# Optimization experiments

Hardware: AMD Instinct MI355X
Metric: run time of the kernel (lower is better)

The kernel has to match this reference:

```python
import jax, jax.numpy as jnp
import numpy as np

D_MODEL = 1024
NUM_HEADS = 16
D_HEAD = D_MODEL // NUM_HEADS


def setup_inputs() -> dict:
    key = jax.random.key(0)
    kx, kq, kk, kv, ko = jax.random.split(key, 5)
    scale = 1.0 / np.sqrt(D_MODEL)
    X = jax.random.normal(kx, (4, 2048, D_MODEL), dtype=jnp.float32)
    # nn.Linear weights stored as [out, in]; we keep that convention.
    W_Q = jax.random.uniform(kq, (D_MODEL, D_MODEL), jnp.float32, -scale, scale)
    W_K = jax.random.uniform(kk, (D_MODEL, D_MODEL), jnp.float32, -scale, scale)
    W_V = jax.random.uniform(kv, (D_MODEL, D_MODEL), jnp.float32, -scale, scale)
    W_O = jax.random.uniform(ko, (D_MODEL, D_MODEL), jnp.float32, -scale, scale)
    return {"X": X, "W_Q": W_Q, "W_K": W_K, "W_V": W_V, "W_O": W_O}


def reference(X, W_Q, W_K, W_V, W_O):
    B, S, D = X.shape
    H, Dh = NUM_HEADS, D_HEAD
    # projections (Linear: x @ W.T)
    Q = (X @ W_Q.T).reshape(B, S, H, Dh).transpose(0, 2, 1, 3)  # [B,H,S,Dh]
    K = (X @ W_K.T).reshape(B, S, H, Dh).transpose(0, 2, 1, 3)
    V = (X @ W_V.T).reshape(B, S, H, Dh).transpose(0, 2, 1, 3)
    scores = jnp.einsum('bhqd,bhkd->bhqk', Q, K) / jnp.sqrt(jnp.float32(Dh))
    causal = jnp.tril(jnp.ones((S, S), dtype=bool))  # True = keep
    scores = jnp.where(causal, scores, -jnp.inf)
    attn = jax.nn.softmax(scores, axis=-1)
    out = jnp.einsum('bhqk,bhkd->bhqd', attn, V)  # [B,H,S,Dh]
    out = out.transpose(0, 2, 1, 3).reshape(B, S, D)
    return out @ W_O.T
```

## Files before the change

kernel.cpp:

```cpp
#include <hip/hip_runtime.h>

#define S_LEN 2048
#define NH 16
#define DH 64
#define DM 1024
#define M_TOK 8192
#define SZX ((size_t)M_TOK * DM)
#define SZW ((size_t)DM * DM)

typedef unsigned short u16;
typedef unsigned int u32;
typedef __attribute__((ext_vector_type(8))) short bf16x8;
typedef __attribute__((ext_vector_type(4))) float f32x4;

__device__ __forceinline__ u16 f2bf(float f) {
  union { float f; u32 u; } v; v.f = f;
  return (u16)((v.u + 0x8000u) >> 16);
}
__device__ __forceinline__ u32 pack_bf2(float x, float y) {
  union { float f; u32 u; } a, b; a.f = x; b.f = y;
  return __builtin_amdgcn_perm(b.u + 0x8000u, a.u + 0x8000u, 0x07060302u);
}
__device__ __forceinline__ float fast_exp2(float x) {
  float r; asm("v_exp_f32 %0, %1" : "=v"(r) : "v"(x)); return r;
}
__device__ __forceinline__ void gload16(const u16* g, u16* l) {
  __builtin_amdgcn_global_load_lds((const __attribute__((address_space(1))) void*)g,
                                   (__attribute__((address_space(3))) void*)l,
                                   16, 0, 0);
}

#define QSCALE 0.18033688f

__global__ __launch_bounds__(256) void cast_all(const float* __restrict__ X,
                                                const float* __restrict__ q,
                                                const float* __restrict__ k,
                                                const float* __restrict__ v,
                                                const float* __restrict__ o,
                                                u16* __restrict__ dst) {
  const int i = (blockIdx.x * 256 + threadIdx.x) * 8;
  const float* src;
  int local;
  if (i < (int)SZX) { src = X; local = i; }
  else {
    const int j = i - (int)SZX;
    const int region = j >> 20;
    src = (region == 0) ? q : (region == 1) ? k : (region == 2) ? v : o;
    local = j & ((1 << 20) - 1);
  }
  const float4 a = *(const float4*)(src + local);
  const float4 b = *(const float4*)(src + local + 4);
  uint4 r;
  r.x = pack_bf2(a.x, a.y); r.y = pack_bf2(a.z, a.w);
  r.z = pack_bf2(b.x, b.y); r.w = pack_bf2(b.z, b.w);
  *(uint4*)(dst + i) = r;
}

template<int MODE, bool SW>
__device__ __forceinline__ void gemm_body(const u16* __restrict__ A,
                                          const u16* __restrict__ Bw,
                                          void* __restrict__ Cv,
                                          u16* __restrict__ As,
                                          u16* __restrict__ Bs) {
  const int tid = threadIdx.x;
  const int lane = tid & 63;
  const int wave = tid >> 6;
  const int col = lane & 15, quad = lane >> 4;
  const int wm = (wave & 1) * 64, wn = (wave >> 1) * 64;
  const int m_blk = blockIdx.x * 128, n_blk = blockIdx.y * 128;

  const int srow = tid >> 3;
  const int skg = (tid & 7) ^ (srow & 7);
  const u16* Ag = A + (size_t)(m_blk + srow) * DM + skg * 8;
  const u16* Bg = Bw + (size_t)(n_blk + srow) * DM + skg * 8;

  f32x4 acc[4][4];
#pragma unroll
  for (int i = 0; i < 4; ++i)
#pragma unroll
    for (int j = 0; j < 4; ++j) acc[i][j] = (f32x4){0.f, 0.f, 0.f, 0.f};

  const int c0 = (quad ^ (col & 7)) * 8;
  const int c1 = c0 ^ 32;

  for (int k0 = 0; k0 < DM; k0 += 64) {
#pragma unroll
    for (int i = 0; i < 4; ++i) {
      gload16(Ag + (size_t)(32 * i) * DM + k0, &As[tid * 8 + i * 2048]);
      gload16(Bg + (size_t)(32 * i) * DM + k0, &Bs[tid * 8 + i * 2048]);
    }
    __syncthreads();
    bf16x8 af[4], bf[4];
#pragma unroll
    for (int i = 0; i < 4; ++i)
      af[i] = *(const bf16x8*)&As[(wm + i * 16 + col) * 64 + c0];
#pragma unroll
    for (int j = 0; j < 4; ++j)
      bf[j] = *(const bf16x8*)&Bs[(wn + j * 16 + col) * 64 + c0];
#pragma unroll
    for (int i = 0; i < 4; ++i)
#pragma unroll
      for (int j = 0; j < 4; ++j)
        acc[i][j] = SW
          ? __builtin_amdgcn_mfma_f32_16x16x32_bf16(bf[j], af[i], acc[i][j], 0, 0, 0)
          : __builtin_amdgcn_mfma_f32_16x16x32_bf16(af[i], bf[j], acc[i][j], 0, 0, 0);
#pragma unroll
    for (int i = 0; i < 4; ++i)
      af[i] = *(const bf16x8*)&As[(wm + i * 16 + col) * 64 + c1];
#pragma unroll
    for (int j = 0; j < 4; ++j)
      bf[j] = *(const bf16x8*)&Bs[(wn + j * 16 + col) * 64 + c1];
#pragma unroll
    for (int i = 0; i < 4; ++i)
#pragma unroll
      for (int j = 0; j < 4; ++j)
        acc[i][j] = SW
          ? __builtin_amdgcn_mfma_f32_16x16x32_bf16(bf[j], af[i], acc[i][j], 0, 0, 0)
          : __builtin_amdgcn_mfma_f32_16x16x32_bf16(af[i], bf[j], acc[i][j], 0, 0, 0);
    __syncthreads();
  }

  if (MODE == 0 && SW) {
    const int which = n_blk >> 10;
    const float sc = (which == 0) ? QSCALE : 1.0f;
    u16* dst = (u16*)Cv + (size_t)which * SZX;
    const int h = ((n_blk + wn) & 1023) >> 6;
#pragma unroll
    for (int i = 0; i < 4; ++i) {
      const int m = m_blk + wm + i * 16 + col;
      const int b = m >> 11, s = m & 2047;
      const size_t rowb = ((size_t)(b * NH + h) * S_LEN + s) * DH;
#pragma unroll
      for (int j = 0; j < 4; ++j) {
        const int dh0 = j * 16 + quad * 4;
        uint2 pk;
        pk.x = pack_bf2(acc[i][j][0] * sc, acc[i][j][1] * sc);
        pk.y = pack_bf2(acc[i][j][2] * sc, acc[i][j][3] * sc);
        *(uint2*)&dst[rowb + dh0] = pk;
      }
    }
  } else if (MODE == 0) {
#pragma unroll
    for (int i = 0; i < 4; ++i) {
#pragma unroll
      for (int j = 0; j < 4; ++j) {
        const int n = n_blk + wn + j * 16 + col;
        const int nn = n & 1023;
        const int h = nn >> 6, dh = nn & 63;
        u16* dst = (u16*)Cv + (size_t)2 * SZX;
        const int m0 = m_blk + wm + i * 16 + quad * 4;
        const int b = m0 >> 11;
        uint2 pk;
        pk.x = pack_bf2(acc[i][j][0], acc[i][j][1]);
        pk.y = pack_bf2(acc[i][j][2], acc[i][j][3]);
        *(uint2*)&dst[((size_t)((b * NH + h) * DH + dh)) * S_LEN + (m0 & 2047)] = pk;
      }
    }
  } else {
#pragma unroll
    for (int i = 0; i < 4; ++i) {
      const int m = m_blk + wm + i * 16 + col;
#pragma unroll
      for (int j = 0; j < 4; ++j) {
        const int n0 = n_blk + wn + j * 16 + quad * 4;
        float4 v;
        v.x = acc[i][j][0]; v.y = acc[i][j][1];
        v.z = acc[i][j][2]; v.w = acc[i][j][3];
        *(float4*)&((float*)Cv)[(size_t)m * DM + n0] = v;
      }
    }
  }
}

template<int MODE>
__global__ __launch_bounds__(256) void gemm128(const u16* __restrict__ A,
                                               const u16* __restrict__ Bw,
                                               void* __restrict__ Cv) {
  __shared__ __align__(16) u16 As[128 * 64];
  __shared__ __align__(16) u16 Bs[128 * 64];
  if (MODE == 0) {
    if ((blockIdx.y * 128) >> 10 == 2) gemm_body<0, false>(A, Bw, Cv, As, Bs);
    else                               gemm_body<0, true >(A, Bw, Cv, As, Bs);
  } else {
    gemm_body<1, true>(A, Bw, Cv, As, Bs);
  }
}

template<bool DIAG_L>
__device__ __forceinline__ void stepM(const u16* __restrict__ Ksb,
                                      const u16* __restrict__ Vsb,
                                      u16* __restrict__ Pw,
                                      bf16x8 qH0, bf16x8 qH1,
                                      bf16x8 qL0, bf16x8 qL1,
                                      f32x4& lH, f32x4* oH,
                                      f32x4& lL, f32x4* oL,
                                      f32x4 zero4, bf16x8 ones,
                                      int c0, int c1, int col, int quad,
                                      int q_l) {
  const int colc = col & 7;
  f32x4 sH[4], sL[4];
#pragma unroll
  for (int t = 0; t < 4; ++t) {
    const int row = (t * 16 + col) * 64;
    const bf16x8 kf0 = *(const bf16x8*)&Ksb[row + c0];
    const bf16x8 kf1 = *(const bf16x8*)&Ksb[row + c1];
    f32x4 z = __builtin_amdgcn_mfma_f32_16x16x32_bf16(kf0, qH0, zero4, 0, 0, 0);
    sH[t] = __builtin_amdgcn_mfma_f32_16x16x32_bf16(kf1, qH1, z, 0, 0, 0);
    f32x4 y = __builtin_amdgcn_mfma_f32_16x16x32_bf16(kf0, qL0, zero4, 0, 0, 0);
    sL[t] = __builtin_amdgcn_mfma_f32_16x16x32_bf16(kf1, qL1, y, 0, 0, 0);
  }
#pragma unroll
  for (int t = 0; t < 4; ++t)
#pragma unroll
    for (int r = 0; r < 4; ++r) {
      sH[t][r] = fast_exp2(sH[t][r]);
      if (DIAG_L && (t * 16 + quad * 4 + r) > q_l) sL[t][r] = -1e30f;
      sL[t][r] = fast_exp2(sL[t][r]);
    }
#pragma unroll
  for (int t = 0; t < 4; ++t) {
    uint2 pk;
    pk.x = pack_bf2(sH[t][0], sH[t][1]);
    pk.y = pack_bf2(sH[t][2], sH[t][3]);
    const int pg = (((t * 2) + (quad >> 1)) ^ colc) * 8 + (quad & 1) * 4;
    *(uint2*)&Pw[col * 64 + pg] = pk;
  }
  const bf16x8 pfH0 = *(const bf16x8*)&Pw[col * 64 + ((quad ^ colc) * 8)];
  const bf16x8 pfH1 = *(const bf16x8*)&Pw[col * 64 + (((4 + quad) ^ colc) * 8)];
#pragma unroll
  for (int t = 0; t < 4; ++t) {
    uint2 pk;
    pk.x = pack_bf2(sL[t][0], sL[t][1]);
    pk.y = pack_bf2(sL[t][2], sL[t][3]);
    const int pg = (((t * 2) + (quad >> 1)) ^ colc) * 8 + (quad & 1) * 4;
    *(uint2*)&Pw[col * 64 + pg] = pk;
  }
  const bf16x8 pfL0 = *(const bf16x8*)&Pw[col * 64 + ((quad ^ colc) * 8)];
  const bf16x8 pfL1 = *(const bf16x8*)&Pw[col * 64 + (((4 + quad) ^ colc) * 8)];
  lH = __builtin_amdgcn_mfma_f32_16x16x32_bf16(ones, pfH0, lH, 0, 0, 0);
  lH = __builtin_amdgcn_mfma_f32_16x16x32_bf16(ones, pfH1, lH, 0, 0, 0);
  lL = __builtin_amdgcn_mfma_f32_16x16x32_bf16(ones, pfL0, lL, 0, 0, 0);
  lL = __builtin_amdgcn_mfma_f32_16x16x32_bf16(ones, pfL1, lL, 0, 0, 0);
#pragma unroll
  for (int t = 0; t < 4; ++t) {
    const int row = (t * 16 + col) * 64;
    const bf16x8 vf0 = *(const bf16x8*)&Vsb[row + c0];
    const bf16x8 vf1 = *(const bf16x8*)&Vsb[row + c1];
    oH[t] = __builtin_amdgcn_mfma_f32_16x16x32_bf16(vf0, pfH0, oH[t], 0, 0, 0);
    oH[t] = __builtin_amdgcn_mfma_f32_16x16x32_bf16(vf1, pfH1, oH[t], 0, 0, 0);
    oL[t] = __builtin_amdgcn_mfma_f32_16x16x32_bf16(vf0, pfL0, oL[t], 0, 0, 0);
    oL[t] = __builtin_amdgcn_mfma_f32_16x16x32_bf16(vf1, pfL1, oL[t], 0, 0, 0);
  }
}

template<bool DIAG_H>
__device__ __forceinline__ void stepS(const u16* __restrict__ Ksb,
                                      const u16* __restrict__ Vsb,
                                      u16* __restrict__ Pw,
                                      bf16x8 qH0, bf16x8 qH1,
                                      f32x4& lH, f32x4* oH,
                                      f32x4 zero4, bf16x8 ones,
                                      int c0, int c1, int col, int quad,
                                      int q_l) {
  const int colc = col & 7;
  f32x4 sH[4];
#pragma unroll
  for (int t = 0; t < 4; ++t) {
    const int row = (t * 16 + col) * 64;
    const bf16x8 kf0 = *(const bf16x8*)&Ksb[row + c0];
    const bf16x8 kf1 = *(const bf16x8*)&Ksb[row + c1];
    f32x4 z = __builtin_amdgcn_mfma_f32_16x16x32_bf16(kf0, qH0, zero4, 0, 0, 0);
    sH[t] = __builtin_amdgcn_mfma_f32_16x16x32_bf16(kf1, qH1, z, 0, 0, 0);
  }
#pragma unroll
  for (int t = 0; t < 4; ++t)
#pragma unroll
    for (int r = 0; r < 4; ++r) {
      if (DIAG_H && (t * 16 + quad * 4 + r) > q_l) sH[t][r] = -1e30f;
      sH[t][r] = fast_exp2(sH[t][r]);
    }
#pragma unroll
  for (int t = 0; t < 4; ++t) {
    uint2 pk;
    pk.x = pack_bf2(sH[t][0], sH[t][1]);
    pk.y = pack_bf2(sH[t][2], sH[t][3]);
    const int pg = (((t * 2) + (quad >> 1)) ^ colc) * 8 + (quad & 1) * 4;
    *(uint2*)&Pw[col * 64 + pg] = pk;
  }
  const bf16x8 pf0 = *(const bf16x8*)&Pw[col * 64 + ((quad ^ colc) * 8)];
  const bf16x8 pf1 = *(const bf16x8*)&Pw[col * 64 + (((4 + quad) ^ colc) * 8)];
  lH = __builtin_amdgcn_mfma_f32_16x16x32_bf16(ones, pf0, lH, 0, 0, 0);
  lH = __builtin_amdgcn_mfma_f32_16x16x32_bf16(ones, pf1, lH, 0, 0, 0);
#pragma unroll
  for (int t = 0; t < 4; ++t) {
    const int row = (t * 16 + col) * 64;
    const bf16x8 vf0 = *(const bf16x8*)&Vsb[row + c0];
    const bf16x8 vf1 = *(const bf16x8*)&Vsb[row + c1];
    oH[t] = __builtin_amdgcn_mfma_f32_16x16x32_bf16(vf0, pf0, oH[t], 0, 0, 0);
    oH[t] = __builtin_amdgcn_mfma_f32_16x16x32_bf16(vf1, pf1, oH[t], 0, 0, 0);
  }
}

__global__ __launch_bounds__(256) void attn_kernel(const u16* __restrict__ Qg,
                                                   const u16* __restrict__ Kg,
                                                   const u16* __restrict__ Vtg,
                                                   u16* __restrict__ AO) {
  __shared__ __align__(16) u16 Ks[2][2][64 * 64];
  __shared__ __align__(16) u16 Vs[2][2][64 * 64];
  __shared__ __align__(16) u16 Ps[4][16 * 64];

  const int id = blockIdx.x;
  const int bh = ((id & 7) << 3) | (id >> 6);
  const int slot = (id >> 3) & 7;
  const int tid = threadIdx.x, lane = tid & 63, wave = tid >> 6;
  const int col = lane & 15, quad = lane >> 4;

  const u16* Qb = Qg + (size_t)bh * S_LEN * DH;
  const u16* Kb = Kg + (size_t)bh * S_LEN * DH;
  const u16* Vb = Vtg + (size_t)bh * DH * S_LEN;

  const f32x4 zero4 = (f32x4){0.f, 0.f, 0.f, 0.f};
  const bf16x8 ones = (bf16x8){0x3F80, 0x3F80, 0x3F80, 0x3F80,
                               0x3F80, 0x3F80, 0x3F80, 0x3F80};

  const int sr0 = tid >> 3;
  const int sk0 = (tid & 7) ^ (sr0 & 7);
  const u16* K0 = Kb + (size_t)sr0 * DH + sk0 * 8;
  const u16* K1 = Kb + (size_t)(sr0 + 32) * DH + sk0 * 8;
  const u16* V0 = Vb + (size_t)sr0 * S_LEN + sk0 * 8;
  const u16* V1 = Vb + (size_t)(sr0 + 32) * S_LEN + sk0 * 8;

  const int c0 = (quad ^ (col & 7)) * 8;
  const int c1 = c0 ^ 32;
  const int q_l = wave * 16 + col;
  u16* Pw = &Ps[wave][0];
  const int b = bh >> 4, h = bh & 15;

#define STAGEW(w, nb) do {                                            \
    gload16(K0 + (size_t)(2 * (w)) * 64 * DH,     &Ks[nb][0][tid * 8]);        \
    gload16(K1 + (size_t)(2 * (w)) * 64 * DH,     &Ks[nb][0][2048 + tid * 8]); \
    gload16(K0 + (size_t)(2 * (w) + 1) * 64 * DH, &Ks[nb][1][tid * 8]);        \
    gload16(K1 + (size_t)(2 * (w) + 1) * 64 * DH, &Ks[nb][1][2048 + tid * 8]); \
    gload16(V0 + (2 * (w)) * 64,                  &Vs[nb][0][tid * 8]);        \
    gload16(V1 + (2 * (w)) * 64,                  &Vs[nb][0][2048 + tid * 8]); \
    gload16(V0 + (2 * (w) + 1) * 64,              &Vs[nb][1][tid * 8]);        \
    gload16(V1 + (2 * (w) + 1) * 64,              &Vs[nb][1][2048 + tid * 8]); \
  } while (0)

  for (int pi = 0; pi < 2; ++pi) {
    const int p = pi ? slot : (15 - slot);
    const int qtH = 2 * p + 1;

    const u16* qrowH = Qb + (size_t)(qtH * 64 + wave * 16 + col) * DH + quad * 8;
    const bf16x8 qH0 = *(const bf16x8*)(qrowH);
    const bf16x8 qH1 = *(const bf16x8*)(qrowH + 32);
    const bf16x8 qL0 = *(const bf16x8*)(qrowH - 64 * DH);
    const bf16x8 qL1 = *(const bf16x8*)(qrowH - 64 * DH + 32);

    f32x4 lH = zero4, lL = zero4;
    f32x4 oH[4], oL[4];
#pragma unroll
    for (int t = 0; t < 4; ++t) { oH[t] = zero4; oL[t] = zero4; }

    __syncthreads();
    STAGEW(0, 0);

    for (int w = 0; w < p; ++w) {
      __syncthreads();
      STAGEW(w + 1, (w + 1) & 1);
      stepM<false>(&Ks[w & 1][0][0], &Vs[w & 1][0][0], Pw,
                   qH0, qH1, qL0, qL1, lH, oH, lL, oL,
                   zero4, ones, c0, c1, col, quad, q_l);
      stepM<false>(&Ks[w & 1][1][0], &Vs[w & 1][1][0], Pw,
                   qH0, qH1, qL0, qL1, lH, oH, lL, oL,
                   zero4, ones, c0, c1, col, quad, q_l);
    }
    {
      __syncthreads();
      stepM<true>(&Ks[p & 1][0][0], &Vs[p & 1][0][0], Pw,
                  qH0, qH1, qL0, qL1, lH, oH, lL, oL,
                  zero4, ones, c0, c1, col, quad, q_l);
      stepS<true>(&Ks[p & 1][1][0], &Vs[p & 1][1][0], Pw,
                  qH0, qH1, lH, oH, zero4, ones, c0, c1, col, quad, q_l);
    }

    {
      const float inv = __builtin_amdgcn_rcpf(lH[0]);
      const size_t base = (size_t)(b * S_LEN + qtH * 64 + q_l) * DM + h * DH;
#pragma unroll
      for (int t = 0; t < 4; ++t) {
        uint2 pk;
        pk.x = pack_bf2(oH[t][0] * inv, oH[t][1] * inv);
        pk.y = pack_bf2(oH[t][2] * inv, oH[t][3] * inv);
        *(uint2*)&AO[base + t * 16 + quad * 4] = pk;
      }
    }
    {
      const float inv = __builtin_amdgcn_rcpf(lL[0]);
      const size_t base = (size_t)(b * S_LEN + (qtH - 1) * 64 + q_l) * DM + h * DH;
#pragma unroll
      for (int t = 0; t < 4; ++t) {
        uint2 pk;
        pk.x = pack_bf2(oL[t][0] * inv, oL[t][1] * inv);
        pk.y = pack_bf2(oL[t][2] * inv, oL[t][3] * inv);
        *(uint2*)&AO[base + t * 16 + quad * 4] = pk;
      }
    }
  }
#undef STAGEW
}

extern "C" void kernel_launch(void* const* d_in, const int* in_sizes, int n_in,
                              void* d_out, int out_size, void* d_ws, size_t ws_size,
                              hipStream_t stream) {
  const float* X  = (const float*)d_in[0];
  const float* Wq = (const float*)d_in[1];
  const float* Wk = (const float*)d_in[2];
  const float* Wv = (const float*)d_in[3];
  const float* Wo = (const float*)d_in[4];

  u16* Xb   = (u16*)d_ws;
  u16* Wqkv = Xb + SZX;
  u16* Wob  = Wqkv + 3 * SZW;
  u16* Qb   = Wob + SZW;
  u16* Kb   = Qb + SZX;
  u16* VT   = Kb + SZX;
  u16* AO   = Xb;

  cast_all<<<(int)((SZX + 4 * SZW) / 8 / 256), 256, 0, stream>>>(X, Wq, Wk, Wv, Wo, Xb);

  gemm128<0><<<dim3(M_TOK / 128, 3 * DM / 128), 256, 0, stream>>>(Xb, Wqkv, Qb);

  attn_kernel<<<dim3(512), 256, 0, stream>>>(Qb, Kb, VT, AO);

  gemm128<1><<<dim3(M_TOK / 128, DM / 128), 256, 0, stream>>>(AO, Wob, d_out);
}
```

Measured before the change: 229.9 us.

## Double-buffer GEMM shared-memory tiles to overlap global loads with MFMA

```diff
diff --git a/kernel.cpp b/kernel.cpp
--- a/kernel.cpp
+++ b/kernel.cpp
@@ -7,6 +7,7 @@
 #define M_TOK 8192
 #define SZX ((size_t)M_TOK * DM)
 #define SZW ((size_t)DM * DM)
+#define NT 16
 
 typedef unsigned short u16;
 typedef unsigned int u32;
@@ -83,20 +84,31 @@
   const int c0 = (quad ^ (col & 7)) * 8;
   const int c1 = c0 ^ 32;
 
-  for (int k0 = 0; k0 < DM; k0 += 64) {
-#pragma unroll
-    for (int i = 0; i < 4; ++i) {
-      gload16(Ag + (size_t)(32 * i) * DM + k0, &As[tid * 8 + i * 2048]);
-      gload16(Bg + (size_t)(32 * i) * DM + k0, &Bs[tid * 8 + i * 2048]);
-    }
+#define STG(t) do {                                                       \
+    const int kk_ = (t) * 64;                                             \
+    u16* Ad_ = As + ((t) & 1) * 8192;                                     \
+    u16* Bd_ = Bs + ((t) & 1) * 8192;                                     \
+    _Pragma("unroll")                                                     \
+    for (int i_ = 0; i_ < 4; ++i_) {                                      \
+      gload16(Ag + (size_t)(32 * i_) * DM + kk_, &Ad_[tid * 8 + i_ * 2048]); \
+      gload16(Bg + (size_t)(32 * i_) * DM + kk_, &Bd_[tid * 8 + i_ * 2048]); \
+    }                                                                     \
+  } while (0)
+
+  STG(0);
+#pragma unroll 2
+  for (int t = 0; t < NT; ++t) {
     __syncthreads();
+    if (t + 1 < NT) STG(t + 1);
+    const u16* Ab = As + (t & 1) * 8192;
+    const u16* Bb = Bs + (t & 1) * 8192;
     bf16x8 af[4], bf[4];
 #pragma unroll
     for (int i = 0; i < 4; ++i)
-      af[i] = *(const bf16x8*)&As[(wm + i * 16 + col) * 64 + c0];
+      af[i] = *(const bf16x8*)&Ab[(wm + i * 16 + col) * 64 + c0];
 #pragma unroll
     for (int j = 0; j < 4; ++j)
-      bf[j] = *(const bf16x8*)&Bs[(wn + j * 16 + col) * 64 + c0];
+      bf[j] = *(const bf16x8*)&Bb[(wn + j * 16 + col) * 64 + c0];
 #pragma unroll
     for (int i = 0; i < 4; ++i)
 #pragma unroll
@@ -106,10 +118,10 @@
           : __builtin_amdgcn_mfma_f32_16x16x32_bf16(af[i], bf[j], acc[i][j], 0, 0, 0);
 #pragma unroll
     for (int i = 0; i < 4; ++i)
-      af[i] = *(const bf16x8*)&As[(wm + i * 16 + col) * 64 + c1];
+      af[i] = *(const bf16x8*)&Ab[(wm + i * 16 + col) * 64 + c1];
 #pragma unroll
     for (int j = 0; j < 4; ++j)
-      bf[j] = *(const bf16x8*)&Bs[(wn + j * 16 + col) * 64 + c1];
+      bf[j] = *(const bf16x8*)&Bb[(wn + j * 16 + col) * 64 + c1];
 #pragma unroll
     for (int i = 0; i < 4; ++i)
 #pragma unroll
@@ -117,8 +129,8 @@
         acc[i][j] = SW
           ? __builtin_amdgcn_mfma_f32_16x16x32_bf16(bf[j], af[i], acc[i][j], 0, 0, 0)
           : __builtin_amdgcn_mfma_f32_16x16x32_bf16(af[i], bf[j], acc[i][j], 0, 0, 0);
-    __syncthreads();
-  }
+  }
+#undef STG
 
   if (MODE == 0 && SW) {
     const int which = n_blk >> 10;
@@ -176,13 +188,13 @@
 __global__ __launch_bounds__(256) void gemm128(const u16* __restrict__ A,
                                                const u16* __restrict__ Bw,
                                                void* __restrict__ Cv) {
-  __shared__ __align__(16) u16 As[128 * 64];
-  __shared__ __align__(16) u16 Bs[128 * 64];
+  __shared__ __align__(16) u16 As[2][128 * 64];
+  __shared__ __align__(16) u16 Bs[2][128 * 64];
   if (MODE == 0) {
-    if ((blockIdx.y * 128) >> 10 == 2) gemm_body<0, false>(A, Bw, Cv, As, Bs);
-    else                               gemm_body<0, true >(A, Bw, Cv, As, Bs);
+    if ((blockIdx.y * 128) >> 10 == 2) gemm_body<0, false>(A, Bw, Cv, &As[0][0], &Bs[0][0]);
+    else                               gemm_body<0, true >(A, Bw, Cv, &As[0][0], &Bs[0][0]);
   } else {
-    gemm_body<1, true>(A, Bw, Cv, As, Bs);
+    gemm_body<1, true>(A, Bw, Cv, &As[0][0], &Bs[0][0]);
   }
 }
 
```

Measured after the change: 231.0 us. No clear change (+0.5%).
